# Kernel optimization log

Measured on AMD Instinct MI355X. Metric: run time of the kernel, lower is better.

The kernel has to match this reference:

```python
import jax, jax.numpy as jnp
import numpy as np

N = 10000   # total nodes
I = 1000    # input nodes   [0, I)
F = 8600    # function nodes [I, I+F)
O = 400     # output nodes  [I+F, N)
E = 80000   # edges
C = 16      # channels per function node
LAYERS = 6
B = 64
EPS = 1e-5  # torch LayerNorm default eps


def _build_graph():
    rng = np.random.default_rng(0)
    fn = np.arange(I, I + F)
    out = np.arange(I + F, N)
    n_if, n_fo = 10000, O
    n_ff = E - n_if - n_fo
    # input -> function (every input node appears as src at least once)
    src_if = np.concatenate([np.arange(I), rng.integers(0, I, n_if - I)])
    dst_if = rng.integers(I, I + F, n_if)
    # function -> function (every function node appears as dst at least once)
    src_ff = rng.integers(I, I + F, n_ff)
    dst_ff = np.concatenate([fn, rng.integers(I, I + F, n_ff - F)])
    # function -> output (each output node has exactly one incoming edge)
    src_fo = rng.integers(I, I + F, n_fo)
    dst_fo = out
    src = np.concatenate([src_if, src_ff, src_fo]).astype(np.int32)
    dst = np.concatenate([dst_if, dst_ff, dst_fo]).astype(np.int32)
    return src, dst


def setup_inputs() -> dict:
    key = jax.random.key(0)
    ks = jax.random.split(key, 8)
    src, dst = _build_graph()
    fn_idx = np.arange(I, I + F).astype(np.int32)
    input_edge_mask = (src < I).astype(np.float32)   # edges leaving input nodes
    fn_src_mask = (src >= I).astype(np.float32)      # W3 only has entries for function-node sources
    last_edge = np.zeros(N, dtype=np.int32)
    has = np.zeros(N, dtype=np.float32)
    last_edge[dst] = np.arange(E)
    has[dst] = 1.0
    s = 1.0 / np.sqrt(C)
    return dict(
        x=jax.random.normal(ks[0], (B, N), jnp.float32),
        w1=jax.random.normal(ks[1], (E, C), jnp.float32) * s,            # lin1 nnz: (e, dst(e)*C+c)
        b1=jax.random.normal(ks[2], (N, C), jnp.float32) * 0.01,
        w2=jax.random.normal(ks[3], (F, C, C), jnp.float32) * s,         # lin2: dense CxC per function node
        b2=jax.random.normal(ks[4], (N, C), jnp.float32) * 0.01,
        w3=jax.random.normal(ks[5], (E, C), jnp.float32) * s * fn_src_mask[:, None],  # lin3 nnz: (src(e)*C+c, e)
        b3=jax.random.normal(ks[6], (E,), jnp.float32) * 0.01,
        scale_out=jnp.ones((1, E, 1), jnp.float32),
        bias_out=jnp.zeros((1, E, 1), jnp.float32),
        src=jnp.asarray(src), dst=jnp.asarray(dst), fn_idx=jnp.asarray(fn_idx),
        input_edge_mask=jnp.asarray(input_edge_mask),
        last_edge=jnp.asarray(last_edge), has_edge=jnp.asarray(has),
    )


def _forward(x, w1, b1, w2, b2, w3, b3, scale_out, bias_out,
             src, dst, fn_idx, input_edge_mask, last_edge, has_edge):
    x0 = x[:, src]                                   # node2edge gather: (B, E)
    xe = x0
    m = input_edge_mask[None, :]                     # (1, E)
    for _ in range(LAYERS):                          # eval mode: full depth, no dropout
        x_last = xe
        # lin1 (sparse E -> C*N): scatter-add edge contributions into dst-node channels
        h = jnp.zeros((B, N, C), x.dtype).at[:, dst, :].add(xe[:, :, None] * w1[None])
        h = jax.nn.elu(h + b1)
        # lin2 (block-diagonal CxC over function nodes); other node channels get bias only
        hf = jnp.einsum('bfc,fcd->bfd', h[:, fn_idx], w2)
        h2 = jax.nn.elu(jnp.zeros((B, N, C), x.dtype).at[:, fn_idx, :].set(hf) + b2)
        # lin3 (sparse C*N -> E): gather src-node channels per edge, contract over C
        xe = jnp.einsum('bec,ec->be', h2[:, src], w3) + b3
        xe = xe + x_last                             # residual
        mu = jnp.mean(xe, axis=-1, keepdims=True)    # LayerNorm over E, no affine
        var = jnp.mean((xe - mu) ** 2, axis=-1, keepdims=True)
        xn = (xe - mu) * jax.lax.rsqrt(var + EPS)
        xe = (1.0 - m) * xn + m * x0                 # pin input edges to x0
    xe = scale_out[0, :, 0][None, :] * xe + bias_out[0, :, 0][None, :]
    return xe[:, last_edge] * has_edge[None, :]      # (B, N)


def reference(x, w1, b1, w2, b2, w3, b3, scale_out, bias_out,
              src, dst, fn_idx, input_edge_mask, last_edge, has_edge):
    return _forward(x, w1, b1, w2, b2, w3, b3, scale_out, bias_out,
                    src, dst, fn_idx, input_edge_mask, last_edge, has_edge)
```

## Files before the change

kernel.cpp:

```cpp
#include <hip/hip_runtime.h>
#include <math.h>

#define NN 10000
#define NI 1000
#define NF 8600
#define NE 80000
#define NC 16
#define NB 64
#define NS (NI + NF)
#define NLAYERS 6
#define LN_EPS 1e-5f
#define PF 8

#define LAYER_BLOCKS ((NF + 7) / 8)
#define TILE_BLOCKS ((NN + 63) / 64)

typedef float f32x4 __attribute__((ext_vector_type(4)));

__device__ __forceinline__ float elu_fast(float x) {
    return x > 0.0f ? x : __expf(x) - 1.0f;
}

__global__ __launch_bounds__(256) void k_transpose(const float* __restrict__ x,
                                                   float* __restrict__ xT) {
    __shared__ float t[64][65];
    int n0 = blockIdx.x * 64;
    int lane = threadIdx.x & 63, w = threadIdx.x >> 6;
    int n = n0 + lane;
    for (int bb = w; bb < 64; bb += 4)
        t[bb][lane] = (n < NN) ? x[(size_t)bb * NN + n] : 0.f;
    __syncthreads();
    for (int nn = w; nn < 64; nn += 4) {
        int nw = n0 + nn;
        if (nw < NN) xT[(size_t)nw * 64 + lane] = t[lane][nn];
    }
}

__global__ void k_count(const int* __restrict__ src, const int* __restrict__ dst,
                        int* __restrict__ cs, int* __restrict__ cd) {
    int e = blockIdx.x * blockDim.x + threadIdx.x;
    if (e >= NE) return;
    atomicAdd(&cs[src[e]], 1);
    int d = dst[e];
    if (d >= NI && d < NI + NF) atomicAdd(&cd[d - NI], 1);
}

__global__ void k_scan2(const int* __restrict__ cs, const int* __restrict__ cd,
                        int* __restrict__ rps, int* __restrict__ rpd) {
    __shared__ int tsum[1024];
    const int* cnt; int* rp; int L;
    if (blockIdx.x == 0) { cnt = cs; rp = rps; L = NS; }
    else                 { cnt = cd; rp = rpd; L = NF; }
    int t = threadIdx.x;
    int per = (L + 1023) >> 10;
    int beg = t * per;
    int end = beg + per; if (end > L) end = L;
    int s = 0;
    for (int i = beg; i < end; ++i) s += cnt[i];
    tsum[t] = s;
    __syncthreads();
    for (int off = 1; off < 1024; off <<= 1) {
        int v = (t >= off) ? tsum[t - off] : 0;
        __syncthreads();
        tsum[t] += v;
        __syncthreads();
    }
    int run = (t == 0) ? 0 : tsum[t - 1];
    for (int i = beg; i < end; ++i) { rp[i] = run; run += cnt[i]; }
    if (t == 1023) rp[L] = tsum[1023];
}

__global__ void k_copyoff(const int* __restrict__ rp_s, const int* __restrict__ rp_d,
                          int* __restrict__ off_s, int* __restrict__ off_d,
                          int* __restrict__ foCtr) {
    int i = blockIdx.x * blockDim.x + threadIdx.x;
    if (i < NS) off_s[i] = rp_s[i];
    if (i < NF) off_d[i] = rp_d[i];
    if (i == 0) foCtr[0] = rp_d[NF];
}

__global__ void k_fill(const int* __restrict__ src, const int* __restrict__ dst,
                       int* __restrict__ off_s, int* __restrict__ off_d,
                       int* __restrict__ foCtr,
                       int* __restrict__ el_s, int* __restrict__ el_d,
                       int* __restrict__ posOf) {
    int e = blockIdx.x * blockDim.x + threadIdx.x;
    if (e >= NE) return;
    int p = atomicAdd(&off_s[src[e]], 1);
    el_s[p] = e;
    int d = dst[e];
    int q;
    if (d >= NI && d < NI + NF) {
        q = atomicAdd(&off_d[d - NI], 1);
        el_d[q] = e;
    } else {
        q = atomicAdd(foCtr, 1);
    }
    posOf[e] = q;
}

__global__ void k_permute(const int* __restrict__ src,
                          const float* __restrict__ w1, const float* __restrict__ w3,
                          const float* __restrict__ b3, const float* __restrict__ b2,
                          const int* __restrict__ rp_d,
                          const int* __restrict__ el_d, const int* __restrict__ el_s,
                          const int* __restrict__ posOf,
                          unsigned* __restrict__ pd, unsigned* __restrict__ pe2,
                          float* __restrict__ w1g, float* __restrict__ w3g,
                          float* __restrict__ b3g, float* __restrict__ c3,
                          int* __restrict__ srcS) {
    int k = blockIdx.x * blockDim.x + threadIdx.x;
    if (k >= NE) return;
    {
        int e = el_s[k];
        int s = src[e];
        srcS[k] = s;
        pe2[k] = (unsigned)(posOf[e] * NB);
        float wrow[NC];
        const f32x4* s4 = (const f32x4*)(w3 + (size_t)e * NC);
        ((f32x4*)wrow)[0] = s4[0]; ((f32x4*)wrow)[1] = s4[1];
        ((f32x4*)wrow)[2] = s4[2]; ((f32x4*)wrow)[3] = s4[3];
        f32x4* d4 = (f32x4*)(w3g + (size_t)k * NC);
        d4[0] = ((f32x4*)wrow)[0]; d4[1] = ((f32x4*)wrow)[1];
        d4[2] = ((f32x4*)wrow)[2]; d4[3] = ((f32x4*)wrow)[3];
        float bb = b3[e];
        b3g[k] = bb;
        float cc = 0.f;
        if (s < NI) {
            const float* b2r = b2 + (size_t)s * NC;
            #pragma unroll
            for (int c = 0; c < NC; ++c) {
                float h = b2r[c];
                h = h > 0.f ? h : __expf(h) - 1.0f;
                cc += h * wrow[c];
            }
            cc += bb;
        }
        c3[k] = cc;
    }
    if (k < rp_d[NF]) {
        int e = el_d[k];
        int s = src[e];
        unsigned off = (s < NI) ? (unsigned)(s * NB) : (unsigned)(k * NB);
        pd[k] = (off << 1) | (s < NI ? 0u : 1u);
        const f32x4* s4 = (const f32x4*)(w1 + (size_t)e * NC);
        f32x4* d4 = (f32x4*)(w1g + (size_t)k * NC);
        d4[0] = s4[0]; d4[1] = s4[1]; d4[2] = s4[2]; d4[3] = s4[3];
    }
}

__global__ void k_init_xe(const float* __restrict__ xT, const int* __restrict__ src,
                          const int* __restrict__ posOf, const int* __restrict__ srcS,
                          float* __restrict__ xeD, float* __restrict__ xeS,
                          float* __restrict__ accum) {
    size_t idx = (size_t)blockIdx.x * blockDim.x + threadIdx.x;
    if (idx < (NLAYERS + 1) * 128) {
        float v = 0.f;
        if (idx >= 64 && idx < 128) v = (float)NE * (1.0f - LN_EPS);
        accum[idx] = v;
    }
    size_t tot = (size_t)NE * NB;
    if (idx < tot) {
        int e = (int)(idx >> 6), b = (int)(idx & 63);
        xeD[(size_t)posOf[e] * NB + b] = xT[(size_t)src[e] * NB + b];
    } else if (idx < 2 * tot) {
        size_t i2 = idx - tot;
        int k = (int)(i2 >> 6), b = (int)(i2 & 63);
        xeS[i2] = xT[(size_t)srcS[k] * NB + b];
    }
}

__global__ __launch_bounds__(256) void k_cstats(
    const float* __restrict__ xT, const int* __restrict__ srcS,
    const float* __restrict__ c3, const int* __restrict__ rp_s,
    float* __restrict__ accum)
{
    __shared__ float shs[256], shq[256];
    int lane = threadIdx.x & 63;
    int nIn = __builtin_amdgcn_readfirstlane(rp_s[NI]);
    float ls = 0.f, lq = 0.f;
    for (int k = blockIdx.x * 4 + (threadIdx.x >> 6); k < nIn; k += gridDim.x * 4) {
        float v = xT[(size_t)srcS[k] * NB + lane] + c3[k];
        ls += v; lq += v * v;
    }
    shs[threadIdx.x] = ls; shq[threadIdx.x] = lq;
    __syncthreads();
    int t = threadIdx.x;
    if (t < 64) {
        float ts = shs[t] + shs[64 + t] + shs[128 + t] + shs[192 + t];
        #pragma unroll
        for (int L = 1; L <= NLAYERS; ++L) atomicAdd(&accum[L * 128 + t], ts);
    } else if (t < 128) {
        int l = t - 64;
        float tq = shq[l] + shq[64 + l] + shq[128 + l] + shq[192 + l];
        #pragma unroll
        for (int L = 1; L <= NLAYERS; ++L) atomicAdd(&accum[L * 128 + 64 + l], tq);
    }
}

__global__ __launch_bounds__(512, 4) void k_layer(
    const float* __restrict__ xT,
    const float* __restrict__ xeDR, float* __restrict__ xeDW,
    float* __restrict__ xeS,
    const float* __restrict__ sums, float* __restrict__ sumsOut,
    const float* __restrict__ w1g, const float* __restrict__ b1,
    const float* __restrict__ w2, const float* __restrict__ b2,
    const float* __restrict__ w3g, const float* __restrict__ b3g,
    const int* __restrict__ rp_d, const unsigned* __restrict__ pd,
    const int* __restrict__ rp_s, const unsigned* __restrict__ pe2)
{
    __shared__ float shs[512], shq[512];
    int lane = threadIdx.x & 63;
    int f = __builtin_amdgcn_readfirstlane((int)(blockIdx.x * 8 + (threadIdx.x >> 6)));
    float lsum = 0.f, lsq = 0.f;
    if (f < NF) {
        int n = NI + f;
        const float inv = 1.0f / (float)NE;
        float mu = sums[lane] * inv;
        float rs = rsqrtf(sums[64 + lane] * inv - mu * mu + LN_EPS);

        float acc[NC];
        {
            const f32x4* b1r = (const f32x4*)(b1 + (size_t)n * NC);
            f32x4 a = b1r[0], b = b1r[1], c = b1r[2], d = b1r[3];
            acc[0]=a.x; acc[1]=a.y; acc[2]=a.z; acc[3]=a.w;
            acc[4]=b.x; acc[5]=b.y; acc[6]=b.z; acc[7]=b.w;
            acc[8]=c.x; acc[9]=c.y; acc[10]=c.z; acc[11]=c.w;
            acc[12]=d.x; acc[13]=d.y; acc[14]=d.z; acc[15]=d.w;
        }
        int k0d = __builtin_amdgcn_readfirstlane(rp_d[f]);
        int k1d = __builtin_amdgcn_readfirstlane(rp_d[f + 1]);
        for (int base = k0d; base < k1d; base += PF) {
            int m = k1d - base; if (m > PF) m = PF;
            unsigned pv[PF];
            #pragma unroll
            for (int j = 0; j < PF; ++j) pv[j] = (j < m) ? pd[base + j] : 0u;
            float raw[PF];
            #pragma unroll
            for (int j = 0; j < PF; ++j)
                if (j < m) {
                    const float* bp = (pv[j] & 1u) ? xeDR : xT;
                    raw[j] = bp[(size_t)(pv[j] >> 1) + lane];
                }
            #pragma unroll
            for (int j = 0; j < PF; ++j) {
                if (j < m) {
                    float xv = (pv[j] & 1u) ? (raw[j] - mu) * rs : raw[j];
                    const f32x4* wr = (const f32x4*)(w1g + (size_t)(base + j) * NC);
                    f32x4 a = wr[0], b = wr[1], c = wr[2], d = wr[3];
                    acc[0]  += xv * a.x; acc[1]  += xv * a.y; acc[2]  += xv * a.z; acc[3]  += xv * a.w;
                    acc[4]  += xv * b.x; acc[5]  += xv * b.y; acc[6]  += xv * b.z; acc[7]  += xv * b.w;
                    acc[8]  += xv * c.x; acc[9]  += xv * c.y; acc[10] += xv * c.z; acc[11] += xv * c.w;
                    acc[12] += xv * d.x; acc[13] += xv * d.y; acc[14] += xv * d.z; acc[15] += xv * d.w;
                }
            }
        }

        int k0s = __builtin_amdgcn_readfirstlane(rp_s[n]);
        int k1s = __builtin_amdgcn_readfirstlane(rp_s[n + 1]);
        int m0 = k1s - k0s; if (m0 > PF) m0 = PF;
        unsigned pos0[PF];
        float old0[PF];
        #pragma unroll
        for (int j = 0; j < PF; ++j)
            if (j < m0) pos0[j] = pe2[k0s + j];
        #pragma unroll
        for (int j = 0; j < PF; ++j)
            if (j < m0) old0[j] = xeS[(size_t)(k0s + j) * NB + lane];

        float h[NC];
        #pragma unroll
        for (int c = 0; c < NC; ++c) h[c] = elu_fast(acc[c]);
        float hf[NC];
        {
            const f32x4* b2r = (const f32x4*)(b2 + (size_t)n * NC);
            f32x4 a = b2r[0], b = b2r[1], c = b2r[2], d = b2r[3];
            hf[0]=a.x; hf[1]=a.y; hf[2]=a.z; hf[3]=a.w;
            hf[4]=b.x; hf[5]=b.y; hf[6]=b.z; hf[7]=b.w;
            hf[8]=c.x; hf[9]=c.y; hf[10]=c.z; hf[11]=c.w;
            hf[12]=d.x; hf[13]=d.y; hf[14]=d.z; hf[15]=d.w;
        }
        const float* w2f = w2 + (size_t)f * NC * NC;
        #pragma unroll
        for (int c = 0; c < NC; ++c) {
            const f32x4* w2r = (const f32x4*)(w2f + c * NC);
            f32x4 a = w2r[0], b = w2r[1], cc = w2r[2], d = w2r[3];
            float hc = h[c];
            hf[0]  += hc * a.x;  hf[1]  += hc * a.y;  hf[2]  += hc * a.z;  hf[3]  += hc * a.w;
            hf[4]  += hc * b.x;  hf[5]  += hc * b.y;  hf[6]  += hc * b.z;  hf[7]  += hc * b.w;
            hf[8]  += hc * cc.x; hf[9]  += hc * cc.y; hf[10] += hc * cc.z; hf[11] += hc * cc.w;
            hf[12] += hc * d.x;  hf[13] += hc * d.y;  hf[14] += hc * d.z;  hf[15] += hc * d.w;
        }
        float hv[NC];
        #pragma unroll
        for (int c = 0; c < NC; ++c) hv[c] = elu_fast(hf[c]);

        for (int base = k0s; base < k1s; base += PF) {
            int m = k1s - base; if (m > PF) m = PF;
            unsigned pos[PF];
            float old[PF];
            if (base == k0s) {
                #pragma unroll
                for (int j = 0; j < PF; ++j) { pos[j] = pos0[j]; old[j] = old0[j]; }
            } else {
                #pragma unroll
                for (int j = 0; j < PF; ++j)
                    if (j < m) pos[j] = pe2[base + j];
                #pragma unroll
                for (int j = 0; j < PF; ++j)
                    if (j < m) old[j] = xeS[(size_t)(base + j) * NB + lane];
            }
            #pragma unroll
            for (int j = 0; j < PF; ++j) {
                if (j < m) {
                    const f32x4* wr = (const f32x4*)(w3g + (size_t)(base + j) * NC);
                    f32x4 a = wr[0], b = wr[1], c = wr[2], d = wr[3];
                    float v = b3g[base + j] + (old[j] - mu) * rs;
                    v += hv[0]*a.x + hv[1]*a.y + hv[2]*a.z + hv[3]*a.w;
                    v += hv[4]*b.x + hv[5]*b.y + hv[6]*b.z + hv[7]*b.w;
                    v += hv[8]*c.x + hv[9]*c.y + hv[10]*c.z + hv[11]*c.w;
                    v += hv[12]*d.x + hv[13]*d.y + hv[14]*d.z + hv[15]*d.w;
                    xeS[(size_t)(base + j) * NB + lane] = v;
                    xeDW[(size_t)pos[j] + lane] = v;
                    lsum += v; lsq += v * v;
                }
            }
        }
    }
    shs[threadIdx.x] = lsum; shq[threadIdx.x] = lsq;
    __syncthreads();
    int t = threadIdx.x;
    if (t < 64) {
        float ts = 0.f;
        #pragma unroll
        for (int w = 0; w < 8; ++w) ts += shs[w * 64 + t];
        atomicAdd(&sumsOut[t], ts);
    } else if (t < 128) {
        int l = t - 64;
        float tq = 0.f;
        #pragma unroll
        for (int w = 0; w < 8; ++w) tq += shq[w * 64 + l];
        atomicAdd(&sumsOut[64 + l], tq);
    }
}

__global__ __launch_bounds__(256) void k_out(
    const float* __restrict__ xT, const float* __restrict__ xeF,
    const float* __restrict__ sums,
    const int* __restrict__ src, const int* __restrict__ posOf,
    const float* __restrict__ scale, const float* __restrict__ bias,
    const int* __restrict__ last_edge, const float* __restrict__ has,
    float* __restrict__ out)
{
    __shared__ float t[64][65];
    int n0 = blockIdx.x * 64;
    int lane = threadIdx.x & 63, w = threadIdx.x >> 6;
    const float inv = 1.0f / (float)NE;
    float mu = sums[lane] * inv;
    float rs = rsqrtf(sums[64 + lane] * inv - mu * mu + LN_EPS);
    for (int nn = w; nn < 64; nn += 4) {
        int n = n0 + nn;
        float val = 0.f;
        if (n < NN) {
            int le = last_edge[n];
            int s = src[le];
            float x0v = xT[(size_t)s * NB + lane];
            float xn = (xeF[(size_t)posOf[le] * NB + lane] - mu) * rs;
            float xf = (s < NI) ? x0v : xn;
            val = has[n] * (scale[le] * xf + bias[le]);
        }
        t[nn][lane] = val;
    }
    __syncthreads();
    for (int bb = w; bb < 64; bb += 4) {
        int n = n0 + lane;
        if (n < NN) out[(size_t)bb * NN + n] = t[lane][bb];
    }
}

extern "C" void kernel_launch(void* const* d_in, const int* in_sizes, int n_in,
                              void* d_out, int out_size, void* d_ws, size_t ws_size,
                              hipStream_t stream) {
    const float* x     = (const float*)d_in[0];
    const float* w1    = (const float*)d_in[1];
    const float* b1    = (const float*)d_in[2];
    const float* w2    = (const float*)d_in[3];
    const float* b2    = (const float*)d_in[4];
    const float* w3    = (const float*)d_in[5];
    const float* b3    = (const float*)d_in[6];
    const float* scale = (const float*)d_in[7];
    const float* bias  = (const float*)d_in[8];
    const int*   src   = (const int*)d_in[9];
    const int*   dst   = (const int*)d_in[10];
    const int*   last  = (const int*)d_in[13];
    const float* has   = (const float*)d_in[14];
    float* out = (float*)d_out;

    char* p = (char*)d_ws;
    auto alloc = [&](size_t bytes) {
        char* r = p;
        p += (bytes + 255) & ~(size_t)255;
        return r;
    };
    float* xT    = (float*)alloc((size_t)NN * NB * 4);
    float* xeDA  = (float*)alloc((size_t)NE * NB * 4);
    float* xeDB  = (float*)alloc((size_t)NE * NB * 4);
    float* xeS   = (float*)alloc((size_t)NE * NB * 4);
    float* accum = (float*)alloc((NLAYERS + 1) * 128 * 4);
    float* w1g   = (float*)alloc((size_t)NE * NC * 4);
    float* w3g   = (float*)alloc((size_t)NE * NC * 4);
    float* b3g   = (float*)alloc((size_t)NE * 4);
    float* c3    = (float*)alloc((size_t)NE * 4);
    unsigned* pd  = (unsigned*)alloc((size_t)NE * 4);
    unsigned* pe2 = (unsigned*)alloc((size_t)NE * 4);
    int* rp_s   = (int*)alloc((NS + 1) * 4);
    int* rp_d   = (int*)alloc((NF + 1) * 4);
    int* el_s   = (int*)alloc((size_t)NE * 4);
    int* el_d   = (int*)alloc((size_t)NE * 4);
    int* posOf  = (int*)alloc((size_t)NE * 4);
    int* srcS   = (int*)alloc((size_t)NE * 4);
    int* off_s  = (int*)alloc(NS * 4);
    int* off_d  = (int*)alloc(NF * 4);
    int* cs     = (int*)alloc(NS * 4);
    int* cd     = (int*)alloc(NF * 4);
    int* foCtr  = (int*)alloc(4);

    hipMemsetAsync(cs, 0, NS * 4, stream);
    hipMemsetAsync(cd, 0, NF * 4, stream);
    k_transpose<<<TILE_BLOCKS, 256, 0, stream>>>(x, xT);
    k_count<<<(NE + 255) / 256, 256, 0, stream>>>(src, dst, cs, cd);
    k_scan2<<<2, 1024, 0, stream>>>(cs, cd, rp_s, rp_d);
    k_copyoff<<<(NS + 255) / 256, 256, 0, stream>>>(rp_s, rp_d, off_s, off_d, foCtr);
    k_fill<<<(NE + 255) / 256, 256, 0, stream>>>(src, dst, off_s, off_d, foCtr,
                                                 el_s, el_d, posOf);
    k_permute<<<(NE + 255) / 256, 256, 0, stream>>>(src, w1, w3, b3, b2, rp_d,
                                                    el_d, el_s, posOf,
                                                    pd, pe2, w1g, w3g, b3g, c3, srcS);
    k_init_xe<<<(int)((2 * (size_t)NE * NB + 255) / 256), 256, 0, stream>>>(
        xT, src, posOf, srcS, xeDA, xeS, accum);
    k_cstats<<<128, 256, 0, stream>>>(xT, srcS, c3, rp_s, accum);

    for (int L = 0; L < NLAYERS; ++L) {
        const float* xeDR = (L & 1) ? xeDB : xeDA;
        float*       xeDW = (L & 1) ? xeDA : xeDB;
        k_layer<<<LAYER_BLOCKS, 512, 0, stream>>>(xT, xeDR, xeDW, xeS,
                                                  accum + L * 128, accum + (L + 1) * 128,
                                                  w1g, b1, w2, b2, w3g, b3g,
                                                  rp_d, pd, rp_s, pe2);
    }
    k_out<<<TILE_BLOCKS, 256, 0, stream>>>(xT, xeDA, accum + NLAYERS * 128, src, posOf,
                                           scale, bias, last, has, out);
}
```

Before: 399.2 us.

## Store edge activations and transposed input in fp16, drop source-ordered copy

```diff
diff --git a/kernel.cpp b/kernel.cpp
--- a/kernel.cpp
+++ b/kernel.cpp
@@ -1,4 +1,5 @@
 #include <hip/hip_runtime.h>
+#include <hip/hip_fp16.h>
 #include <math.h>
 
 #define NN 10000
@@ -22,7 +23,7 @@
 }
 
 __global__ __launch_bounds__(256) void k_transpose(const float* __restrict__ x,
-                                                   float* __restrict__ xT) {
+                                                   __half* __restrict__ xTh) {
     __shared__ float t[64][65];
     int n0 = blockIdx.x * 64;
     int lane = threadIdx.x & 63, w = threadIdx.x >> 6;
@@ -32,7 +33,7 @@
     __syncthreads();
     for (int nn = w; nn < 64; nn += 4) {
         int nw = n0 + nn;
-        if (nw < NN) xT[(size_t)nw * 64 + lane] = t[lane][nn];
+        if (nw < NN) xTh[(size_t)nw * 64 + lane] = __float2half_rn(t[lane][nn]);
     }
 }
 
@@ -149,29 +150,22 @@
     }
 }
 
-__global__ void k_init_xe(const float* __restrict__ xT, const int* __restrict__ src,
-                          const int* __restrict__ posOf, const int* __restrict__ srcS,
-                          float* __restrict__ xeD, float* __restrict__ xeS,
-                          float* __restrict__ accum) {
+__global__ void k_init_xe(const __half* __restrict__ xTh, const int* __restrict__ src,
+                          const int* __restrict__ posOf,
+                          __half* __restrict__ xeA, float* __restrict__ accum) {
     size_t idx = (size_t)blockIdx.x * blockDim.x + threadIdx.x;
     if (idx < (NLAYERS + 1) * 128) {
         float v = 0.f;
         if (idx >= 64 && idx < 128) v = (float)NE * (1.0f - LN_EPS);
         accum[idx] = v;
     }
-    size_t tot = (size_t)NE * NB;
-    if (idx < tot) {
-        int e = (int)(idx >> 6), b = (int)(idx & 63);
-        xeD[(size_t)posOf[e] * NB + b] = xT[(size_t)src[e] * NB + b];
-    } else if (idx < 2 * tot) {
-        size_t i2 = idx - tot;
-        int k = (int)(i2 >> 6), b = (int)(i2 & 63);
-        xeS[i2] = xT[(size_t)srcS[k] * NB + b];
-    }
+    if (idx >= (size_t)NE * NB) return;
+    int e = (int)(idx >> 6), b = (int)(idx & 63);
+    xeA[(size_t)posOf[e] * NB + b] = xTh[(size_t)src[e] * NB + b];
 }
 
 __global__ __launch_bounds__(256) void k_cstats(
-    const float* __restrict__ xT, const int* __restrict__ srcS,
+    const __half* __restrict__ xTh, const int* __restrict__ srcS,
     const float* __restrict__ c3, const int* __restrict__ rp_s,
     float* __restrict__ accum)
 {
@@ -180,7 +174,7 @@
     int nIn = __builtin_amdgcn_readfirstlane(rp_s[NI]);
     float ls = 0.f, lq = 0.f;
     for (int k = blockIdx.x * 4 + (threadIdx.x >> 6); k < nIn; k += gridDim.x * 4) {
-        float v = xT[(size_t)srcS[k] * NB + lane] + c3[k];
+        float v = __half2float(xTh[(size_t)srcS[k] * NB + lane]) + c3[k];
         ls += v; lq += v * v;
     }
     shs[threadIdx.x] = ls; shq[threadIdx.x] = lq;
@@ -199,9 +193,8 @@
 }
 
 __global__ __launch_bounds__(512, 4) void k_layer(
-    const float* __restrict__ xT,
-    const float* __restrict__ xeDR, float* __restrict__ xeDW,
-    float* __restrict__ xeS,
+    const __half* __restrict__ xTh,
+    const __half* __restrict__ xeR, __half* __restrict__ xeW,
     const float* __restrict__ sums, float* __restrict__ sumsOut,
     const float* __restrict__ w1g, const float* __restrict__ b1,
     const float* __restrict__ w2, const float* __restrict__ b2,
@@ -239,8 +232,8 @@
             #pragma unroll
             for (int j = 0; j < PF; ++j)
                 if (j < m) {
-                    const float* bp = (pv[j] & 1u) ? xeDR : xT;
-                    raw[j] = bp[(size_t)(pv[j] >> 1) + lane];
+                    const __half* bp = (pv[j] & 1u) ? xeR : xTh;
+                    raw[j] = __half2float(bp[(size_t)(pv[j] >> 1) + lane]);
                 }
             #pragma unroll
             for (int j = 0; j < PF; ++j) {
@@ -266,7 +259,7 @@
             if (j < m0) pos0[j] = pe2[k0s + j];
         #pragma unroll
         for (int j = 0; j < PF; ++j)
-            if (j < m0) old0[j] = xeS[(size_t)(k0s + j) * NB + lane];
+            if (j < m0) old0[j] = __half2float(xeR[(size_t)pos0[j] + lane]);
 
         float h[NC];
         #pragma unroll
@@ -308,7 +301,7 @@
                     if (j < m) pos[j] = pe2[base + j];
                 #pragma unroll
                 for (int j = 0; j < PF; ++j)
-                    if (j < m) old[j] = xeS[(size_t)(base + j) * NB + lane];
+                    if (j < m) old[j] = __half2float(xeR[(size_t)pos[j] + lane]);
             }
             #pragma unroll
             for (int j = 0; j < PF; ++j) {
@@ -320,8 +313,7 @@
                     v += hv[4]*b.x + hv[5]*b.y + hv[6]*b.z + hv[7]*b.w;
                     v += hv[8]*c.x + hv[9]*c.y + hv[10]*c.z + hv[11]*c.w;
                     v += hv[12]*d.x + hv[13]*d.y + hv[14]*d.z + hv[15]*d.w;
-                    xeS[(size_t)(base + j) * NB + lane] = v;
-                    xeDW[(size_t)pos[j] + lane] = v;
+                    xeW[(size_t)pos[j] + lane] = __float2half_rn(v);
                     lsum += v; lsq += v * v;
                 }
             }
@@ -345,7 +337,7 @@
 }
 
 __global__ __launch_bounds__(256) void k_out(
-    const float* __restrict__ xT, const float* __restrict__ xeF,
+    const __half* __restrict__ xTh, const __half* __restrict__ xeF,
     const float* __restrict__ sums,
     const int* __restrict__ src, const int* __restrict__ posOf,
     const float* __restrict__ scale, const float* __restrict__ bias,
@@ -364,8 +356,8 @@
         if (n < NN) {
             int le = last_edge[n];
             int s = src[le];
-            float x0v = xT[(size_t)s * NB + lane];
-            float xn = (xeF[(size_t)posOf[le] * NB + lane] - mu) * rs;
+            float x0v = __half2float(xTh[(size_t)s * NB + lane]);
+            float xn = (__half2float(xeF[(size_t)posOf[le] * NB + lane]) - mu) * rs;
             float xf = (s < NI) ? x0v : xn;
             val = has[n] * (scale[le] * xf + bias[le]);
         }
@@ -402,10 +394,9 @@
         p += (bytes + 255) & ~(size_t)255;
         return r;
     };
-    float* xT    = (float*)alloc((size_t)NN * NB * 4);
-    float* xeDA  = (float*)alloc((size_t)NE * NB * 4);
-    float* xeDB  = (float*)alloc((size_t)NE * NB * 4);
-    float* xeS   = (float*)alloc((size_t)NE * NB * 4);
+    __half* xTh  = (__half*)alloc((size_t)NN * NB * 2);
+    __half* xeA  = (__half*)alloc((size_t)NE * NB * 2);
+    __half* xeB  = (__half*)alloc((size_t)NE * NB * 2);
     float* accum = (float*)alloc((NLAYERS + 1) * 128 * 4);
     float* w1g   = (float*)alloc((size_t)NE * NC * 4);
     float* w3g   = (float*)alloc((size_t)NE * NC * 4);
@@ -427,7 +418,7 @@
 
     hipMemsetAsync(cs, 0, NS * 4, stream);
     hipMemsetAsync(cd, 0, NF * 4, stream);
-    k_transpose<<<TILE_BLOCKS, 256, 0, stream>>>(x, xT);
+    k_transpose<<<TILE_BLOCKS, 256, 0, stream>>>(x, xTh);
     k_count<<<(NE + 255) / 256, 256, 0, stream>>>(src, dst, cs, cd);
     k_scan2<<<2, 1024, 0, stream>>>(cs, cd, rp_s, rp_d);
     k_copyoff<<<(NS + 255) / 256, 256, 0, stream>>>(rp_s, rp_d, off_s, off_d, foCtr);
@@ -436,18 +427,18 @@
     k_permute<<<(NE + 255) / 256, 256, 0, stream>>>(src, w1, w3, b3, b2, rp_d,
                                                     el_d, el_s, posOf,
                                                     pd, pe2, w1g, w3g, b3g, c3, srcS);
-    k_init_xe<<<(int)((2 * (size_t)NE * NB + 255) / 256), 256, 0, stream>>>(
-        xT, src, posOf, srcS, xeDA, xeS, accum);
-    k_cstats<<<128, 256, 0, stream>>>(xT, srcS, c3, rp_s, accum);
+    k_init_xe<<<(int)(((size_t)NE * NB + 255) / 256), 256, 0, stream>>>(xTh, src, posOf,
+                                                                        xeA, accum);
+    k_cstats<<<128, 256, 0, stream>>>(xTh, srcS, c3, rp_s, accum);
 
     for (int L = 0; L < NLAYERS; ++L) {
-        const float* xeDR = (L & 1) ? xeDB : xeDA;
-        float*       xeDW = (L & 1) ? xeDA : xeDB;
-        k_layer<<<LAYER_BLOCKS, 512, 0, stream>>>(xT, xeDR, xeDW, xeS,
+        const __half* xeR = (L & 1) ? xeB : xeA;
+        __half*       xeW = (L & 1) ? xeA : xeB;
+        k_layer<<<LAYER_BLOCKS, 512, 0, stream>>>(xTh, xeR, xeW,
                                                   accum + L * 128, accum + (L + 1) * 128,
                                                   w1g, b1, w2, b2, w3g, b3g,
                                                   rp_d, pd, rp_s, pe2);
     }
-    k_out<<<TILE_BLOCKS, 256, 0, stream>>>(xT, xeDA, accum + NLAYERS * 128, src, posOf,
+    k_out<<<TILE_BLOCKS, 256, 0, stream>>>(xTh, xeA, accum + NLAYERS * 128, src, posOf,
                                            scale, bias, last, has, out);
 }
```

Result: slower. 444.4 us (+11.3%).
